# Kernel tuning notes

Hardware: AMD Instinct MI355X
Metric: run time of the kernel (lower is better)

Reference implementation:

```python
import math
import jax, jax.numpy as jnp
import numpy as np

B, T, C, HS = 8, 2048, 1024, 64

def setup_inputs() -> dict:
    key = jax.random.key(0)
    kx, kq, kk, kv = jax.random.split(key, 4)
    x = jax.random.normal(kx, (B, T, C), dtype=jnp.float32)
    # match nn.Linear init scale roughly: U(-1/sqrt(C), 1/sqrt(C))
    lim = 1.0 / math.sqrt(C)
    Wq = jax.random.uniform(kq, (C, HS), minval=-lim, maxval=lim, dtype=jnp.float32)
    Wk = jax.random.uniform(kk, (C, HS), minval=-lim, maxval=lim, dtype=jnp.float32)
    Wv = jax.random.uniform(kv, (C, HS), minval=-lim, maxval=lim, dtype=jnp.float32)
    return {"x": x, "Wq": Wq, "Wk": Wk, "Wv": Wv}

def reference(x, Wq, Wk, Wv):
    # NOTE: original scales by 1/sqrt(hs) where hs = x.shape[-1] = embd_size,
    # not head_size. Faithfully reproduced.
    Tlen = x.shape[1]
    scale = 1.0 / math.sqrt(x.shape[-1])
    q = jnp.einsum('btc,ch->bth', x, Wq)
    k = jnp.einsum('btc,ch->bth', x, Wk)
    v = jnp.einsum('btc,ch->bth', x, Wv)
    wei = jnp.einsum('bth,bsh->bts', q, k) * scale  # [B,T,T]
    causal = jnp.tril(jnp.ones((Tlen, Tlen), dtype=bool))
    wei = jnp.where(causal, wei, -jnp.inf)
    wei = jax.nn.softmax(wei, axis=-1)
    # dropout p=0.0 -> identity
    out = jnp.einsum('bts,bsh->bth', wei, v)  # [B,T,HS]
    return out
```

## Files before the change

kernel.cpp:

```cpp
#include <hip/hip_runtime.h>
#include <hip/hip_bf16.h>


#define T_SEQ 2048
#define C_DIM 1024
#define HS 64
#define BT 16384

typedef short s8v __attribute__((ext_vector_type(8)));
typedef float f4v __attribute__((ext_vector_type(4)));

__device__ inline unsigned short f2bf(float f) {
  union { float f; unsigned u; } a; a.f = f;
  unsigned r = a.u + 0x7fffu + ((a.u >> 16) & 1u);
  return (unsigned short)(r >> 16);
}

__device__ inline s8v cvt8(float4 v0, float4 v1) {
  union { __hip_bfloat162 h; unsigned u; } c0, c1, c2, c3;
  c0.h = __float22bfloat162_rn(make_float2(v0.x, v0.y));
  c1.h = __float22bfloat162_rn(make_float2(v0.z, v0.w));
  c2.h = __float22bfloat162_rn(make_float2(v1.x, v1.y));
  c3.h = __float22bfloat162_rn(make_float2(v1.z, v1.w));
  union { unsigned u[4]; s8v v; } r;
  r.u[0] = c0.u; r.u[1] = c1.u; r.u[2] = c2.u; r.u[3] = c3.u;
  return r.v;
}

__device__ inline void gl_lds16(const void* g, unsigned char* lds_base,
                                unsigned uniform_byte_off) {
  __builtin_amdgcn_global_load_lds(
      (const __attribute__((address_space(1))) unsigned int*)g,
      (__attribute__((address_space(3))) unsigned int*)(lds_base + uniform_byte_off),
      16, 0, 0);
}

__global__ __launch_bounds__(256) void wt_kernel(
    const float* __restrict__ Wq, const float* __restrict__ Wk,
    const float* __restrict__ Wv, unsigned short* __restrict__ wt) {
  __shared__ float tile[64][65];
  const int bid = blockIdx.x;
  const int mat = bid >> 4, kt = bid & 15;
  const float* W = (mat == 0) ? Wq : ((mat == 1) ? Wk : Wv);
  const int t = threadIdx.x;
  const int n = t & 63, kr = t >> 6;
#pragma unroll
  for (int j = 0; j < 16; ++j) {
    const int kl = j * 4 + kr;
    tile[kl][n] = W[(kt * 64 + kl) * HS + n];
  }
  __syncthreads();
  const int n2 = t >> 2, kp = t & 3;
  unsigned int* orow =
      (unsigned int*)(wt + (size_t)(mat * 64 + n2) * C_DIM + kt * 64);
#pragma unroll
  for (int i = 0; i < 8; ++i) {
    const int k0 = kp * 16 + i * 2;
    unsigned int lo = f2bf(tile[k0][n2]);
    unsigned int hi = f2bf(tile[k0 + 1][n2]);
    orow[kp * 8 + i] = lo | (hi << 16);
  }
}

__global__ __launch_bounds__(256) void qkv_kernel(
    const float* __restrict__ x, const unsigned short* __restrict__ wt,
    unsigned short* __restrict__ qws, unsigned short* __restrict__ kws,
    unsigned short* __restrict__ vtws) {
  __shared__ unsigned char abuf[2][8192];
  __shared__ unsigned char bbuf[2][24576];

  const int tid  = threadIdx.x;
  const int wv   = tid >> 6;
  const int lane = tid & 63;
  const int m    = lane & 15;
  const int quad = lane >> 4;
  const int row0 = blockIdx.x * 32;
  const int mh   = wv >> 1;
  const int ng   = (wv & 1) * 6;

  f4v acc[6];
#pragma unroll
  for (int j = 0; j < 6; ++j) acc[j] = (f4v)0.0f;

  const unsigned au = (unsigned)__builtin_amdgcn_readfirstlane(tid & 192) << 4;

  const float* agp[2];
#pragma unroll
  for (int j = 0; j < 2; ++j) {
    const int s = tid + j * 256;
    const int r = s >> 4, p = (s & 15) ^ (r & 15);
    agp[j] = x + (size_t)(row0 + r) * C_DIM + p * 4;
  }
  const unsigned short* bgp[6];
#pragma unroll
  for (int j = 0; j < 6; ++j) {
    const int s = tid + j * 256;
    const int n = s >> 3, p = (s & 7) ^ (n & 7);
    bgp[j] = wt + (size_t)n * C_DIM + p * 8;
  }

  int aoff[2][2];
#pragma unroll
  for (int c = 0; c < 2; ++c)
#pragma unroll
    for (int t = 0; t < 2; ++t)
      aoff[c][t] = (((mh * 16 + m) * 16) + ((c * 8 + 2 * quad + t) ^ m)) << 4;
  int boff[6][2];
#pragma unroll
  for (int j = 0; j < 6; ++j) {
    const int n = (ng + j) * 16 + m;
#pragma unroll
    for (int c = 0; c < 2; ++c)
      boff[j][c] = (n * 8 + ((c * 4 + quad) ^ (n & 7))) << 4;
  }

#define STAGE(buf, kk)                                                       \
  do {                                                                       \
    _Pragma("unroll") for (int j = 0; j < 2; ++j)                            \
        gl_lds16(agp[j] + (kk), abuf[buf], au + (unsigned)(j * 4096));       \
    _Pragma("unroll") for (int j = 0; j < 6; ++j)                            \
        gl_lds16(bgp[j] + (kk), bbuf[buf], au + (unsigned)(j * 4096));       \
  } while (0)

  STAGE(0, 0);
  for (int it = 0; it < 16; ++it) {
    __syncthreads();
    if (it < 15) STAGE((it + 1) & 1, (it + 1) * 64);
    const unsigned char* aB = abuf[it & 1];
    const unsigned char* bB = bbuf[it & 1];
#pragma unroll
    for (int c = 0; c < 2; ++c) {
      float4 xa = *(const float4*)(aB + aoff[c][0]);
      float4 xb = *(const float4*)(aB + aoff[c][1]);
      s8v a = cvt8(xa, xb);
#pragma unroll
      for (int j = 0; j < 6; ++j) {
        s8v b = *(const s8v*)(bB + boff[j][c]);
        acc[j] = __builtin_amdgcn_mfma_f32_16x16x32_bf16(a, b, acc[j], 0, 0, 0);
      }
    }
  }
#undef STAGE

  const float qscale = 1.4426950408889634f / 32.0f;
#pragma unroll
  for (int j = 0; j < 6; ++j) {
    const int nt = ng + j;
    const int mat = nt >> 2, ct = nt & 3;
    const int col = ct * 16 + m;
#pragma unroll
    for (int r = 0; r < 4; ++r) {
      const int row = row0 + mh * 16 + quad * 4 + r;
      const float v = acc[j][r];
      if (mat == 0) {
        qws[row * HS + col] = f2bf(v * qscale);
      } else if (mat == 1) {
        kws[row * HS + col] = f2bf(v);
      } else {
        const int bb = row >> 11, t = row & 2047;
        vtws[(bb * HS + col) * T_SEQ + t] = f2bf(v);
      }
    }
  }
}

union AttnSh {
  unsigned short p[8][16 * 76];
  struct { float mo[4][16][64]; float ml[4][16]; } m;
};

__global__ __launch_bounds__(512, 2) void attn_kernel(
    const unsigned short* __restrict__ qws, const unsigned short* __restrict__ kws,
    const unsigned short* __restrict__ vtws, float* __restrict__ out) {
  __shared__ unsigned char kbuf[2][8192];
  __shared__ unsigned char vbuf[2][8192];
  __shared__ AttnSh sh;

  const int tid  = threadIdx.x;
  const int wv   = tid >> 6;
  const int lane = tid & 63;
  const int m    = lane & 15;
  const int quad = lane >> 4;
  const int b    = blockIdx.x & 7;
  const int qt   = 31 - (blockIdx.x >> 3);
  const int r0   = qt * 64;
  const int qsub = wv >> 1;
  const int par  = wv & 1;
  const int rw   = r0 + qsub * 16;
  const int gr0  = b * T_SEQ + rw;

  s8v aq0 = *(const s8v*)&qws[(size_t)(gr0 + m) * HS + quad * 8];
  s8v aq1 = *(const s8v*)&qws[(size_t)(gr0 + m) * HS + 32 + quad * 8];

  float li[4] = {0.f, 0.f, 0.f, 0.f};
  f4v o[4];
#pragma unroll
  for (int i = 0; i < 4; ++i) o[i] = (f4v)0.0f;

  const int nst    = qt + 1;
  const int mylast = (rw + 15) >> 6;
  const int qrow_base = rw + quad * 4;
  unsigned short* pl = sh.p[wv];

  const unsigned short* kbase = kws + (size_t)b * T_SEQ * HS;
  const unsigned short* vbase = vtws + (size_t)b * HS * T_SEQ;

  const int rt = tid >> 3;
  const int pt = (tid & 7) ^ (rt & 7);
  const unsigned au = (unsigned)__builtin_amdgcn_readfirstlane(tid & 448) << 4;

  int fo[4][2];
#pragma unroll
  for (int ns = 0; ns < 4; ++ns)
#pragma unroll
    for (int c = 0; c < 2; ++c)
      fo[ns][c] = ((ns * 16 + m) * 8 + ((c * 4 + quad) ^ (m & 7))) << 4;

#define STAGEKV(buf, st)                                                     \
  do {                                                                       \
    const int s0_ = (st) * 64;                                               \
    gl_lds16(kbase + (size_t)(s0_ + rt) * HS + pt * 8, kbuf[buf], au);       \
    gl_lds16(vbase + (size_t)rt * T_SEQ + s0_ + pt * 8, vbuf[buf], au);      \
  } while (0)

  STAGEKV(0, 0);
  for (int st = 0; st < nst; ++st) {
    __syncthreads();
    if (st + 1 < nst) STAGEKV((st + 1) & 1, st + 1);
    if ((st & 1) == par && st <= mylast) {
      const unsigned char* kB = kbuf[st & 1];
      const unsigned char* vB = vbuf[st & 1];
      const int s0 = st * 64;

      f4v sacc[4];
#pragma unroll
      for (int ns = 0; ns < 4; ++ns) {
        f4v t = (f4v)0.0f;
        t = __builtin_amdgcn_mfma_f32_16x16x32_bf16(
            aq0, *(const s8v*)(kB + fo[ns][0]), t, 0, 0, 0);
        t = __builtin_amdgcn_mfma_f32_16x16x32_bf16(
            aq1, *(const s8v*)(kB + fo[ns][1]), t, 0, 0, 0);
        sacc[ns] = t;
      }

#pragma unroll
      for (int ns = 0; ns < 4; ++ns) {
        const int scol = s0 + ns * 16 + m;
#pragma unroll
        for (int r = 0; r < 4; ++r) {
          const float p = (scol > qrow_base + r) ? 0.f
                          : __builtin_amdgcn_exp2f(sacc[ns][r]);
          li[r] += p;
          pl[(quad * 4 + r) * 76 + ns * 16 + m] = f2bf(p);
        }
      }

      s8v ap0 = *(const s8v*)&pl[m * 76 + quad * 8];
      s8v ap1 = *(const s8v*)&pl[m * 76 + 32 + quad * 8];
#pragma unroll
      for (int hn = 0; hn < 4; ++hn) {
        o[hn] = __builtin_amdgcn_mfma_f32_16x16x32_bf16(
            ap0, *(const s8v*)(vB + fo[hn][0]), o[hn], 0, 0, 0);
        o[hn] = __builtin_amdgcn_mfma_f32_16x16x32_bf16(
            ap1, *(const s8v*)(vB + fo[hn][1]), o[hn], 0, 0, 0);
      }
    }
  }

#pragma unroll
  for (int r = 0; r < 4; ++r) {
    float s = li[r];
    s += __shfl_xor(s, 1); s += __shfl_xor(s, 2);
    s += __shfl_xor(s, 4); s += __shfl_xor(s, 8);
    li[r] = s;
  }

  __syncthreads();

  if (par == 1) {
#pragma unroll
    for (int hn = 0; hn < 4; ++hn)
#pragma unroll
      for (int r = 0; r < 4; ++r)
        sh.m.mo[qsub][quad * 4 + r][hn * 16 + m] = o[hn][r];
    if (m == 0) {
#pragma unroll
      for (int r = 0; r < 4; ++r) sh.m.ml[qsub][quad * 4 + r] = li[r];
    }
  }
  __syncthreads();
  if (par == 0) {
#pragma unroll
    for (int r = 0; r < 4; ++r) {
      const int row = quad * 4 + r;
      const float inv = 1.0f / (li[r] + sh.m.ml[qsub][row]);
#pragma unroll
      for (int hn = 0; hn < 4; ++hn) {
        const float v = o[hn][r] + sh.m.mo[qsub][row][hn * 16 + m];
        out[(size_t)(gr0 + row) * HS + hn * 16 + m] = v * inv;
      }
    }
  }
}

extern "C" void kernel_launch(void* const* d_in, const int* in_sizes, int n_in,
                              void* d_out, int out_size, void* d_ws, size_t ws_size,
                              hipStream_t stream) {
  const float* x  = (const float*)d_in[0];
  const float* Wq = (const float*)d_in[1];
  const float* Wk = (const float*)d_in[2];
  const float* Wv = (const float*)d_in[3];
  float* out = (float*)d_out;

  unsigned short* qws  = (unsigned short*)d_ws;
  unsigned short* kws  = qws + (size_t)BT * HS;
  unsigned short* vtws = kws + (size_t)BT * HS;
  unsigned short* wt   = vtws + (size_t)BT * HS;

  wt_kernel<<<dim3(48), dim3(256), 0, stream>>>(Wq, Wk, Wv, wt);
  qkv_kernel<<<dim3(BT / 32), dim3(256), 0, stream>>>(x, wt, qws, kws, vtws);
  attn_kernel<<<dim3(256), dim3(512), 0, stream>>>(qws, kws, vtws, out);
}
```

Measured before the change: 158.5 us.

## Deepen QKV load pipeline to 4-slot ring and split attention into smaller blocks

The QKV projection kernel now streams K in 32-wide chunks through a 4-slot LDS ring with three loads in flight, using explicit vmcnt waits plus a barrier instead of plain double buffering. The attention kernel moves to 256-thread blocks covering 32 query rows, doubling the grid for better load balance across CUs. Row sums are now computed with an extra MFMA against a ones vector rather than scalar adds and shuffles, and the causal mask is only applied on the diagonal tile. The costs are more barriers per K step in QKV, a slightly larger wasted load at the end of the ring, and duplicated K/V staging per block in attention.

```diff
diff --git a/kernel.cpp b/kernel.cpp
--- a/kernel.cpp
+++ b/kernel.cpp
@@ -62,12 +62,11 @@
   }
 }
 
-__global__ __launch_bounds__(256) void qkv_kernel(
+__global__ __launch_bounds__(256, 2) void qkv_kernel(
     const float* __restrict__ x, const unsigned short* __restrict__ wt,
     unsigned short* __restrict__ qws, unsigned short* __restrict__ kws,
     unsigned short* __restrict__ vtws) {
-  __shared__ unsigned char abuf[2][8192];
-  __shared__ unsigned char bbuf[2][24576];
+  __shared__ unsigned char ring[4][16384];
 
   const int tid  = threadIdx.x;
   const int wv   = tid >> 6;
@@ -84,63 +83,55 @@
 
   const unsigned au = (unsigned)__builtin_amdgcn_readfirstlane(tid & 192) << 4;
 
-  const float* agp[2];
-#pragma unroll
-  for (int j = 0; j < 2; ++j) {
+  const int ar = tid >> 3;
+  const int apt = (tid & 7) ^ (ar & 7);
+  const float* agp = x + (size_t)(row0 + ar) * C_DIM + apt * 4;
+  const unsigned short* bgp[3];
+#pragma unroll
+  for (int j = 0; j < 3; ++j) {
     const int s = tid + j * 256;
-    const int r = s >> 4, p = (s & 15) ^ (r & 15);
-    agp[j] = x + (size_t)(row0 + r) * C_DIM + p * 4;
-  }
-  const unsigned short* bgp[6];
-#pragma unroll
-  for (int j = 0; j < 6; ++j) {
-    const int s = tid + j * 256;
-    const int n = s >> 3, p = (s & 7) ^ (n & 7);
+    const int n = s >> 2, p = (s & 3) ^ (n & 3);
     bgp[j] = wt + (size_t)n * C_DIM + p * 8;
   }
 
-  int aoff[2][2];
-#pragma unroll
-  for (int c = 0; c < 2; ++c)
-#pragma unroll
-    for (int t = 0; t < 2; ++t)
-      aoff[c][t] = (((mh * 16 + m) * 16) + ((c * 8 + 2 * quad + t) ^ m)) << 4;
-  int boff[6][2];
+  int aoff[2];
+#pragma unroll
+  for (int t = 0; t < 2; ++t)
+    aoff[t] = (((mh * 16 + m) * 8) + ((2 * quad + t) ^ (m & 7))) << 4;
+  int boff[6];
 #pragma unroll
   for (int j = 0; j < 6; ++j) {
     const int n = (ng + j) * 16 + m;
-#pragma unroll
-    for (int c = 0; c < 2; ++c)
-      boff[j][c] = (n * 8 + ((c * 4 + quad) ^ (n & 7))) << 4;
-  }
-
-#define STAGE(buf, kk)                                                       \
+    boff[j] = (n * 4 + (quad ^ (n & 3))) << 4;
+  }
+
+#define STAGE(slot, kk)                                                      \
   do {                                                                       \
-    _Pragma("unroll") for (int j = 0; j < 2; ++j)                            \
-        gl_lds16(agp[j] + (kk), abuf[buf], au + (unsigned)(j * 4096));       \
-    _Pragma("unroll") for (int j = 0; j < 6; ++j)                            \
-        gl_lds16(bgp[j] + (kk), bbuf[buf], au + (unsigned)(j * 4096));       \
+    gl_lds16(agp + (kk), ring[slot], au);                                    \
+    _Pragma("unroll") for (int j = 0; j < 3; ++j)                            \
+        gl_lds16(bgp[j] + (kk), ring[slot] + 4096,                           \
+                 au + (unsigned)(j * 4096));                                 \
   } while (0)
 
   STAGE(0, 0);
-  for (int it = 0; it < 16; ++it) {
-    __syncthreads();
-    if (it < 15) STAGE((it + 1) & 1, (it + 1) * 64);
-    const unsigned char* aB = abuf[it & 1];
-    const unsigned char* bB = bbuf[it & 1];
-#pragma unroll
-    for (int c = 0; c < 2; ++c) {
-      float4 xa = *(const float4*)(aB + aoff[c][0]);
-      float4 xb = *(const float4*)(aB + aoff[c][1]);
-      s8v a = cvt8(xa, xb);
-#pragma unroll
-      for (int j = 0; j < 6; ++j) {
-        s8v b = *(const s8v*)(bB + boff[j][c]);
-        acc[j] = __builtin_amdgcn_mfma_f32_16x16x32_bf16(a, b, acc[j], 0, 0, 0);
-      }
+  STAGE(1, 32);
+  STAGE(2, 64);
+  for (int it = 0; it < 32; ++it) {
+    asm volatile("s_waitcnt vmcnt(8)\n\ts_barrier" ::: "memory");
+    STAGE((it + 3) & 3, ((it + 3) & 31) * 32);
+    const unsigned char* aB = ring[it & 3];
+    const unsigned char* bB = ring[it & 3] + 4096;
+    float4 xa = *(const float4*)(aB + aoff[0]);
+    float4 xb = *(const float4*)(aB + aoff[1]);
+    s8v a = cvt8(xa, xb);
+#pragma unroll
+    for (int j = 0; j < 6; ++j) {
+      s8v b = *(const s8v*)(bB + boff[j]);
+      acc[j] = __builtin_amdgcn_mfma_f32_16x16x32_bf16(a, b, acc[j], 0, 0, 0);
     }
   }
 #undef STAGE
+  asm volatile("s_waitcnt vmcnt(0)" ::: "memory");
 
   const float qscale = 1.4426950408889634f / 32.0f;
 #pragma unroll
@@ -165,11 +156,11 @@
 }
 
 union AttnSh {
-  unsigned short p[8][16 * 76];
-  struct { float mo[4][16][64]; float ml[4][16]; } m;
+  unsigned short p[4][16 * 76];
+  struct { float mo[2][16][64]; float ml[2][16]; } m;
 };
 
-__global__ __launch_bounds__(512, 2) void attn_kernel(
+__global__ __launch_bounds__(256, 2) void attn_kernel(
     const unsigned short* __restrict__ qws, const unsigned short* __restrict__ kws,
     const unsigned short* __restrict__ vtws, float* __restrict__ out) {
   __shared__ unsigned char kbuf[2][8192];
@@ -182,32 +173,40 @@
   const int m    = lane & 15;
   const int quad = lane >> 4;
   const int b    = blockIdx.x & 7;
-  const int qt   = 31 - (blockIdx.x >> 3);
-  const int r0   = qt * 64;
+  const int qt   = 63 - (blockIdx.x >> 3);
   const int qsub = wv >> 1;
   const int par  = wv & 1;
-  const int rw   = r0 + qsub * 16;
+  const int rw   = qt * 32 + qsub * 16;
   const int gr0  = b * T_SEQ + rw;
 
   s8v aq0 = *(const s8v*)&qws[(size_t)(gr0 + m) * HS + quad * 8];
   s8v aq1 = *(const s8v*)&qws[(size_t)(gr0 + m) * HS + 32 + quad * 8];
 
-  float li[4] = {0.f, 0.f, 0.f, 0.f};
-  f4v o[4];
+  s8v ones;
+#pragma unroll
+  for (int i = 0; i < 8; ++i) ones[i] = (short)0x3F80;
+
+  f4v o[4], o4;
 #pragma unroll
   for (int i = 0; i < 4; ++i) o[i] = (f4v)0.0f;
-
-  const int nst    = qt + 1;
-  const int mylast = (rw + 15) >> 6;
+  o4 = (f4v)0.0f;
+
+  const int nst = (32 * qt + 95) >> 6;
+  const int t_d = (rw + 15) >> 6;
   const int qrow_base = rw + quad * 4;
   unsigned short* pl = sh.p[wv];
 
   const unsigned short* kbase = kws + (size_t)b * T_SEQ * HS;
   const unsigned short* vbase = vtws + (size_t)b * HS * T_SEQ;
 
-  const int rt = tid >> 3;
-  const int pt = (tid & 7) ^ (rt & 7);
-  const unsigned au = (unsigned)__builtin_amdgcn_readfirstlane(tid & 448) << 4;
+  int srow[2], spart[2];
+#pragma unroll
+  for (int j = 0; j < 2; ++j) {
+    const int s = tid + j * 256;
+    srow[j] = s >> 3;
+    spart[j] = (s & 7) ^ (srow[j] & 7);
+  }
+  const unsigned au = (unsigned)__builtin_amdgcn_readfirstlane(tid & 192) << 4;
 
   int fo[4][2];
 #pragma unroll
@@ -219,15 +218,19 @@
 #define STAGEKV(buf, st)                                                     \
   do {                                                                       \
     const int s0_ = (st) * 64;                                               \
-    gl_lds16(kbase + (size_t)(s0_ + rt) * HS + pt * 8, kbuf[buf], au);       \
-    gl_lds16(vbase + (size_t)rt * T_SEQ + s0_ + pt * 8, vbuf[buf], au);      \
+    _Pragma("unroll") for (int j = 0; j < 2; ++j) {                          \
+      gl_lds16(kbase + (size_t)(s0_ + srow[j]) * HS + spart[j] * 8,          \
+               kbuf[buf], au + (unsigned)(j * 4096));                        \
+      gl_lds16(vbase + (size_t)srow[j] * T_SEQ + s0_ + spart[j] * 8,         \
+               vbuf[buf], au + (unsigned)(j * 4096));                        \
+    }                                                                        \
   } while (0)
 
   STAGEKV(0, 0);
   for (int st = 0; st < nst; ++st) {
     __syncthreads();
     if (st + 1 < nst) STAGEKV((st + 1) & 1, st + 1);
-    if ((st & 1) == par && st <= mylast) {
+    if ((st & 1) == par && st <= t_d) {
       const unsigned char* kB = kbuf[st & 1];
       const unsigned char* vB = vbuf[st & 1];
       const int s0 = st * 64;
@@ -243,15 +246,23 @@
         sacc[ns] = t;
       }
 
-#pragma unroll
-      for (int ns = 0; ns < 4; ++ns) {
-        const int scol = s0 + ns * 16 + m;
-#pragma unroll
-        for (int r = 0; r < 4; ++r) {
-          const float p = (scol > qrow_base + r) ? 0.f
-                          : __builtin_amdgcn_exp2f(sacc[ns][r]);
-          li[r] += p;
-          pl[(quad * 4 + r) * 76 + ns * 16 + m] = f2bf(p);
+      if (st < t_d) {
+#pragma unroll
+        for (int ns = 0; ns < 4; ++ns)
+#pragma unroll
+          for (int r = 0; r < 4; ++r)
+            pl[(quad * 4 + r) * 76 + ns * 16 + m] =
+                f2bf(__builtin_amdgcn_exp2f(sacc[ns][r]));
+      } else {
+#pragma unroll
+        for (int ns = 0; ns < 4; ++ns) {
+          const int scol = s0 + ns * 16 + m;
+#pragma unroll
+          for (int r = 0; r < 4; ++r) {
+            const float p = (scol > qrow_base + r) ? 0.f
+                            : __builtin_amdgcn_exp2f(sacc[ns][r]);
+            pl[(quad * 4 + r) * 76 + ns * 16 + m] = f2bf(p);
+          }
         }
       }
 
@@ -264,15 +275,9 @@
         o[hn] = __builtin_amdgcn_mfma_f32_16x16x32_bf16(
             ap1, *(const s8v*)(vB + fo[hn][1]), o[hn], 0, 0, 0);
       }
-    }
-  }
-
-#pragma unroll
-  for (int r = 0; r < 4; ++r) {
-    float s = li[r];
-    s += __shfl_xor(s, 1); s += __shfl_xor(s, 2);
-    s += __shfl_xor(s, 4); s += __shfl_xor(s, 8);
-    li[r] = s;
+      o4 = __builtin_amdgcn_mfma_f32_16x16x32_bf16(ap0, ones, o4, 0, 0, 0);
+      o4 = __builtin_amdgcn_mfma_f32_16x16x32_bf16(ap1, ones, o4, 0, 0, 0);
+    }
   }
 
   __syncthreads();
@@ -285,7 +290,7 @@
         sh.m.mo[qsub][quad * 4 + r][hn * 16 + m] = o[hn][r];
     if (m == 0) {
 #pragma unroll
-      for (int r = 0; r < 4; ++r) sh.m.ml[qsub][quad * 4 + r] = li[r];
+      for (int r = 0; r < 4; ++r) sh.m.ml[qsub][quad * 4 + r] = o4[r];
     }
   }
   __syncthreads();
@@ -293,7 +298,7 @@
 #pragma unroll
     for (int r = 0; r < 4; ++r) {
       const int row = quad * 4 + r;
-      const float inv = 1.0f / (li[r] + sh.m.ml[qsub][row]);
+      const float inv = 1.0f / (o4[r] + sh.m.ml[qsub][row]);
 #pragma unroll
       for (int hn = 0; hn < 4; ++hn) {
         const float v = o[hn][r] + sh.m.mo[qsub][row][hn * 16 + m];
@@ -319,5 +324,5 @@
 
   wt_kernel<<<dim3(48), dim3(256), 0, stream>>>(Wq, Wk, Wv, wt);
   qkv_kernel<<<dim3(BT / 32), dim3(256), 0, stream>>>(x, wt, qws, kws, vtws);
-  attn_kernel<<<dim3(256), dim3(512), 0, stream>>>(qws, kws, vtws, out);
-}
+  attn_kernel<<<dim3(512), dim3(256), 0, stream>>>(qws, kws, vtws, out);
+}
```

Measured after the change: 158.2 us. No clear change (-0.2%).
